# Kernel optimization log

Hardware: AMD Instinct MI355X
Metric: run time of the kernel (lower is better)

The kernel has to match this reference:

```python
import jax, jax.numpy as jnp
import numpy as np

TOPK = 20
EPS = 1e-5  # torch BatchNorm1d default eps


def _segment_softmax(logits, seg, num_segments):
    m = jax.ops.segment_max(logits, seg, num_segments=num_segments)
    e = jnp.exp(logits - m[seg])
    s = jax.ops.segment_sum(e, seg, num_segments=num_segments)
    return e / (s[seg] + 1e-16)


def _forward(data, emb, W_lin, att_i, att_j, att_em_i, att_em_j, bias_gnn,
             W_ff, b_ff, bn1_g, bn1_b, bn2_g, bn2_b, W_out, b_out):
    B, N, F = data.shape
    H, D = att_i.shape
    BN = B * N
    x = data.reshape(BN, F)

    # --- dynamic top-k cosine-similarity graph (original detaches embeddings) ---
    w = jax.lax.stop_gradient(emb)
    nrm = jnp.linalg.norm(w, axis=-1, keepdims=True)  # (N,1)
    cos = (w @ w.T) / (nrm * nrm.T)                   # (N,N)
    _, topk_idx = jax.lax.top_k(cos, TOPK)            # (N,K)

    src = topk_idx.reshape(-1)                        # j (source of message)
    tgt = jnp.repeat(jnp.arange(N), TOPK)             # i (target)
    off = (jnp.arange(B) * N)[:, None]                # batch the edge list
    src_b = (src[None, :] + off).reshape(-1)          # (B*N*K,)
    tgt_b = (tgt[None, :] + off).reshape(-1)
    # remove_self_loops then add_self_loops: mask topk self-edges, append loops
    self_mask = src_b == tgt_b
    loops = jnp.arange(BN)
    src_all = jnp.concatenate([src_b, loops])         # (E,)
    tgt_all = jnp.concatenate([tgt_b, loops])
    dead = jnp.concatenate([self_mask, jnp.zeros(BN, dtype=bool)])

    # --- GraphLayer: GAT-style attention with node embeddings in the keys ---
    xh = (x @ W_lin).reshape(BN, H, D)                # lin(x), per head
    emb_full = jnp.tile(emb, (B, 1))                  # (BN, D) repeated per batch
    # per-node attention scores; key_i = [x_i || emb_i] . [att_i || att_em_i]
    score_i = jnp.einsum('nhd,hd->nh', xh, att_i) + emb_full @ att_em_i.T  # (BN,H)
    score_j = jnp.einsum('nhd,hd->nh', xh, att_j) + emb_full @ att_em_j.T
    alpha = score_i[tgt_all] + score_j[src_all]       # (E,H)
    alpha = jax.nn.leaky_relu(alpha, 0.2)
    alpha = jnp.where(dead[:, None], -1e30, alpha)    # drop removed self-edges
    alpha = _segment_softmax(alpha, tgt_all, BN)      # softmax over in-edges of i
    msgs = xh[src_all] * alpha[:, :, None]            # (E,H,D)
    agg = jax.ops.segment_sum(msgs, tgt_all, num_segments=BN)  # (BN,H,D)
    out = agg.reshape(BN, H * D) + bias_gnn           # concat heads + bias

    # --- GNNLayer head: linear -> BatchNorm1d (train stats) -> relu ---
    out = out @ W_ff + b_ff                           # (BN, D)
    mu = out.mean(0)
    var = out.var(0)
    out = (out - mu) / jnp.sqrt(var + EPS) * bn1_g + bn1_b
    out = jax.nn.relu(out)

    # --- multiply by embeddings, channelwise BN, relu (dropout: eval = identity) ---
    h = out.reshape(B, N, D) * emb[None]              # (B,N,D)
    mu2 = h.mean(axis=(0, 1))
    var2 = h.var(axis=(0, 1))
    h = (h - mu2) / jnp.sqrt(var2 + EPS) * bn2_g + bn2_b
    h = jax.nn.relu(h)

    # --- OutLayer (layer_num=1): single linear per node ---
    return h @ W_out + b_out                          # (B, N, out_win)


def setup_inputs() -> dict:
    key = jax.random.key(0)
    ks = jax.random.split(key, 12)
    B, N, F, D, H, OW = 16, 2000, 128, 64, 4, 200
    s = 0.05
    return {
        'data': jax.random.normal(ks[0], (B, N, F), jnp.float32),
        'emb': jax.random.normal(ks[1], (N, D), jnp.float32),
        'W_lin': jax.random.normal(ks[2], (F, H * D), jnp.float32) * s,
        'att_i': jax.random.normal(ks[3], (H, D), jnp.float32) * s,
        'att_j': jax.random.normal(ks[4], (H, D), jnp.float32) * s,
        'att_em_i': jax.random.normal(ks[5], (H, D), jnp.float32) * s,
        'att_em_j': jax.random.normal(ks[6], (H, D), jnp.float32) * s,
        'bias_gnn': jnp.zeros((H * D,), jnp.float32),
        'W_ff': jax.random.normal(ks[7], (H * D, D), jnp.float32) * s,
        'b_ff': jnp.zeros((D,), jnp.float32),
        'bn1_g': jnp.ones((D,), jnp.float32),
        'bn1_b': jnp.zeros((D,), jnp.float32),
        'bn2_g': jnp.ones((D,), jnp.float32),
        'bn2_b': jnp.zeros((D,), jnp.float32),
        'W_out': jax.random.normal(ks[8], (D, OW), jnp.float32) * s,
        'b_out': jnp.zeros((OW,), jnp.float32),
    }


def reference(data, emb, W_lin, att_i, att_j, att_em_i, att_em_j, bias_gnn,
              W_ff, b_ff, bn1_g, bn1_b, bn2_g, bn2_b, W_out, b_out):
    return _forward(data, emb, W_lin, att_i, att_j, att_em_i, att_em_j, bias_gnn,
                    W_ff, b_ff, bn1_g, bn1_b, bn2_g, bn2_b, W_out, b_out)
```

## Files before the change

### kernel.cpp

```cpp
#include <hip/hip_runtime.h>
#include <math.h>

#define B_   16
#define N_   2000
#define F_   128
#define D_   64
#define H_   4
#define OW_  200
#define K_   20
#define BN_  (B_*N_)
#define HD_  (H_*D_)
#define EPS_ 1e-5f
#define NP_  2048

__global__ __launch_bounds__(256) void k_prep(const float* __restrict__ emb,
                                              const float* __restrict__ biasg,
                                              const float* __restrict__ Wff,
                                              const float* __restrict__ bff,
                                              float* __restrict__ nrm,
                                              float* __restrict__ embT,
                                              float* __restrict__ bias2) {
    const int t = threadIdx.x, b = blockIdx.x;
    const int idx = b * 256 + t;
    {
        int k = idx >> 11, j = idx & (NP_ - 1);
        embT[idx] = (j < N_) ? emb[(size_t)j * D_ + k] : 0.f;
    }
    if (b < 8) {
        int i = idx;
        if (i < N_) {
            const float* e = emb + (size_t)i * D_;
            float s = 0.f;
            #pragma unroll
            for (int d = 0; d < D_; ++d) s += e[d] * e[d];
            nrm[i] = sqrtf(s);
        } else if (i < NP_) {
            nrm[i] = 1.f;
        }
    }
    if (b == 8 && t < D_) {
        float s = bff[t];
        for (int c = 0; c < HD_; ++c) s = fmaf(biasg[c], Wff[(size_t)c * D_ + t], s);
        bias2[t] = s;
    }
}

__global__ __launch_bounds__(256) void k_cos(const float* __restrict__ emb,
                                             const float* __restrict__ embT,
                                             const float* __restrict__ nrm,
                                             float* __restrict__ cosm) {
    const int t    = threadIdx.x;
    const int i0   = blockIdx.y * 16;
    const int r0   = (t >> 6) * 4;
    const int lane = t & 63;
    const int j4   = blockIdx.x * 256 + lane * 4;

    __shared__ float eL[16 * D_];
    for (int idx = t; idx < 16 * D_; idx += 256)
        eL[idx] = emb[(size_t)i0 * D_ + idx];
    __syncthreads();

    float acc[4][4];
    #pragma unroll
    for (int r = 0; r < 4; ++r)
        #pragma unroll
        for (int cc = 0; cc < 4; ++cc) acc[r][cc] = 0.f;

    for (int k4 = 0; k4 < D_; k4 += 4) {
        float es[4][4];
        #pragma unroll
        for (int r = 0; r < 4; ++r) {
            float4 ev = *(const float4*)&eL[(r0 + r) * D_ + k4];
            es[r][0] = ev.x; es[r][1] = ev.y; es[r][2] = ev.z; es[r][3] = ev.w;
        }
        #pragma unroll
        for (int kk = 0; kk < 4; ++kk) {
            float4 b = *(const float4*)&embT[(size_t)(k4 + kk) * NP_ + j4];
            #pragma unroll
            for (int r = 0; r < 4; ++r) {
                acc[r][0] = fmaf(es[r][kk], b.x, acc[r][0]);
                acc[r][1] = fmaf(es[r][kk], b.y, acc[r][1]);
                acc[r][2] = fmaf(es[r][kk], b.z, acc[r][2]);
                acc[r][3] = fmaf(es[r][kk], b.w, acc[r][3]);
            }
        }
    }

    float4 nj = *(const float4*)&nrm[j4];
    #pragma unroll
    for (int r = 0; r < 4; ++r) {
        float ni = nrm[i0 + r0 + r];
        float4 o;
        o.x = acc[r][0] / (ni * nj.x);
        o.y = acc[r][1] / (ni * nj.y);
        o.z = acc[r][2] / (ni * nj.z);
        o.w = acc[r][3] / (ni * nj.w);
        *(float4*)&cosm[(size_t)(i0 + r0 + r) * NP_ + j4] = o;
    }
}

__device__ __forceinline__ unsigned long long kmax64(unsigned long long a,
                                                     unsigned long long b) {
    return a > b ? a : b;
}

__global__ __launch_bounds__(256) void k_sel(const float* __restrict__ cosm,
                                             int* __restrict__ topk) {
    const int t    = threadIdx.x;
    const int lane = t & 63;
    const int i    = blockIdx.x * 4 + (t >> 6);
    const float* row = cosm + (size_t)i * NP_;

    unsigned long long key[32];
    #pragma unroll
    for (int m = 0; m < 8; ++m) {
        float4 b = *(const float4*)&row[m * 256 + lane * 4];
        float vv[4] = {b.x, b.y, b.z, b.w};
        #pragma unroll
        for (int q = 0; q < 4; ++q) {
            const int s = m * 4 + q;
            const int j = m * 256 + lane * 4 + q;
            unsigned int x  = __float_as_uint(vv[q]);
            unsigned int mv = (x & 0x80000000u) ? ~x : (x | 0x80000000u);
            unsigned long long kk =
                ((unsigned long long)mv << 32) | (unsigned int)(NP_ - 1 - j);
            key[s] = (j < N_) ? kk : 0ull;
        }
    }

    unsigned long long loc;
    {
        unsigned long long l1[16];
        #pragma unroll
        for (int s = 0; s < 16; ++s) l1[s] = kmax64(key[s], key[s + 16]);
        unsigned long long l2[8];
        #pragma unroll
        for (int s = 0; s < 8; ++s) l2[s] = kmax64(l1[s], l1[s + 8]);
        unsigned long long l3[4];
        #pragma unroll
        for (int s = 0; s < 4; ++s) l3[s] = kmax64(l2[s], l2[s + 4]);
        loc = kmax64(kmax64(l3[0], l3[2]), kmax64(l3[1], l3[3]));
    }

    for (int k = 0; k < K_; ++k) {
        unsigned long long w = loc;
        #pragma unroll
        for (int off = 1; off < 64; off <<= 1)
            w = kmax64(w, __shfl_xor(w, off, 64));

        if (lane == 0)
            topk[i * K_ + k] = (NP_ - 1) - (int)(unsigned int)(w & 0xFFFFFFFFu);

        #pragma unroll
        for (int s = 0; s < 32; ++s)
            if (key[s] == w) key[s] = 0ull;
        {
            unsigned long long l1[16];
            #pragma unroll
            for (int s = 0; s < 16; ++s) l1[s] = kmax64(key[s], key[s + 16]);
            unsigned long long l2[8];
            #pragma unroll
            for (int s = 0; s < 8; ++s) l2[s] = kmax64(l1[s], l1[s + 8]);
            unsigned long long l3[4];
            #pragma unroll
            for (int s = 0; s < 4; ++s) l3[s] = kmax64(l2[s], l2[s + 4]);
            loc = kmax64(kmax64(l3[0], l3[2]), kmax64(l3[1], l3[3]));
        }
    }
}

__global__ __launch_bounds__(256) void k_lin(const float* __restrict__ x,
                                             const float* __restrict__ Wlin,
                                             const float* __restrict__ emb,
                                             const float* __restrict__ atti,
                                             const float* __restrict__ attj,
                                             const float* __restrict__ attei,
                                             const float* __restrict__ attej,
                                             const float* __restrict__ Wff,
                                             float* __restrict__ yh,
                                             float* __restrict__ si,
                                             float* __restrict__ sj) {
    const int t  = threadIdx.x;
    const int n0 = blockIdx.x * 16;
    const int i0 = n0 % N_;
    const int r0 = (t >> 6) * 4;
    const int lane = t & 63;
    const int c4 = lane * 4;

    __shared__ float xL[16 * F_];
    __shared__ float xhL[16 * HD_];

    for (int idx = t; idx < 16 * F_; idx += 256)
        xL[idx] = x[(size_t)n0 * F_ + idx];
    __syncthreads();

    float acc[4][4];
    #pragma unroll
    for (int r = 0; r < 4; ++r)
        #pragma unroll
        for (int cc = 0; cc < 4; ++cc) acc[r][cc] = 0.f;

    for (int k4 = 0; k4 < F_; k4 += 4) {
        float xs[4][4];
        #pragma unroll
        for (int r = 0; r < 4; ++r) {
            float4 xv = *(const float4*)&xL[(r0 + r) * F_ + k4];
            xs[r][0] = xv.x; xs[r][1] = xv.y; xs[r][2] = xv.z; xs[r][3] = xv.w;
        }
        #pragma unroll
        for (int kk = 0; kk < 4; ++kk) {
            float4 w = *(const float4*)&Wlin[(size_t)(k4 + kk) * HD_ + c4];
            #pragma unroll
            for (int r = 0; r < 4; ++r) {
                acc[r][0] = fmaf(xs[r][kk], w.x, acc[r][0]);
                acc[r][1] = fmaf(xs[r][kk], w.y, acc[r][1]);
                acc[r][2] = fmaf(xs[r][kk], w.z, acc[r][2]);
                acc[r][3] = fmaf(xs[r][kk], w.w, acc[r][3]);
            }
        }
    }

    #pragma unroll
    for (int r = 0; r < 4; ++r) {
        float4 o; o.x = acc[r][0]; o.y = acc[r][1]; o.z = acc[r][2]; o.w = acc[r][3];
        *(float4*)&xhL[(r0 + r) * HD_ + c4] = o;
    }

    {
        const int h  = lane >> 4;
        const int de = 4 * (t & 15);
        float4 ai4  = *(const float4*)&atti[c4];
        float4 aj4  = *(const float4*)&attj[c4];
        float4 aei4 = *(const float4*)&attei[c4];
        float4 aej4 = *(const float4*)&attej[c4];
        #pragma unroll
        for (int r = 0; r < 4; ++r) {
            float4 e4 = *(const float4*)&emb[(size_t)(i0 + r0 + r) * D_ + de];
            float vi = acc[r][0] * ai4.x + e4.x * aei4.x
                     + acc[r][1] * ai4.y + e4.y * aei4.y
                     + acc[r][2] * ai4.z + e4.z * aei4.z
                     + acc[r][3] * ai4.w + e4.w * aei4.w;
            float vj = acc[r][0] * aj4.x + e4.x * aej4.x
                     + acc[r][1] * aj4.y + e4.y * aej4.y
                     + acc[r][2] * aj4.z + e4.z * aej4.z
                     + acc[r][3] * aj4.w + e4.w * aej4.w;
            #pragma unroll
            for (int off = 1; off < 16; off <<= 1) {
                vi += __shfl_xor(vi, off);
                vj += __shfl_xor(vj, off);
            }
            if ((t & 15) == 0) {
                si[(size_t)(n0 + r0 + r) * H_ + h] = vi;
                sj[(size_t)(n0 + r0 + r) * H_ + h] = vj;
            }
        }
    }
    __syncthreads();

    {
        const int h  = c4 >> 6;
        const int d4 = c4 & 63;
        float ya[4][4];
        #pragma unroll
        for (int r = 0; r < 4; ++r)
            #pragma unroll
            for (int cc = 0; cc < 4; ++cc) ya[r][cc] = 0.f;

        for (int k4 = 0; k4 < D_; k4 += 4) {
            float wf[4][4];
            #pragma unroll
            for (int kk = 0; kk < 4; ++kk) {
                float4 w = *(const float4*)&Wff[(size_t)(h * D_ + k4 + kk) * D_ + d4];
                wf[kk][0] = w.x; wf[kk][1] = w.y; wf[kk][2] = w.z; wf[kk][3] = w.w;
            }
            #pragma unroll
            for (int r = 0; r < 4; ++r) {
                float4 xv = *(const float4*)&xhL[(r0 + r) * HD_ + h * D_ + k4];
                ya[r][0] = fmaf(xv.x, wf[0][0], ya[r][0]);
                ya[r][1] = fmaf(xv.x, wf[0][1], ya[r][1]);
                ya[r][2] = fmaf(xv.x, wf[0][2], ya[r][2]);
                ya[r][3] = fmaf(xv.x, wf[0][3], ya[r][3]);
                ya[r][0] = fmaf(xv.y, wf[1][0], ya[r][0]);
                ya[r][1] = fmaf(xv.y, wf[1][1], ya[r][1]);
                ya[r][2] = fmaf(xv.y, wf[1][2], ya[r][2]);
                ya[r][3] = fmaf(xv.y, wf[1][3], ya[r][3]);
                ya[r][0] = fmaf(xv.z, wf[2][0], ya[r][0]);
                ya[r][1] = fmaf(xv.z, wf[2][1], ya[r][1]);
                ya[r][2] = fmaf(xv.z, wf[2][2], ya[r][2]);
                ya[r][3] = fmaf(xv.z, wf[2][3], ya[r][3]);
                ya[r][0] = fmaf(xv.w, wf[3][0], ya[r][0]);
                ya[r][1] = fmaf(xv.w, wf[3][1], ya[r][1]);
                ya[r][2] = fmaf(xv.w, wf[3][2], ya[r][2]);
                ya[r][3] = fmaf(xv.w, wf[3][3], ya[r][3]);
            }
        }
        #pragma unroll
        for (int r = 0; r < 4; ++r) {
            float4 o; o.x = ya[r][0]; o.y = ya[r][1]; o.z = ya[r][2]; o.w = ya[r][3];
            *(float4*)&yh[(size_t)(n0 + r0 + r) * HD_ + c4] = o;
        }
    }
}

#define RA_ 8
__global__ __launch_bounds__(256) void k_attn(const float* __restrict__ yh,
                                              const float* __restrict__ si,
                                              const float* __restrict__ sj,
                                              const int* __restrict__ topk,
                                              const float* __restrict__ bias2,
                                              float* __restrict__ out2) {
    const int t   = threadIdx.x;
    const int nwg = BN_ / RA_;
    const int swz = (blockIdx.x & 7) * (nwg >> 3) + (blockIdx.x >> 3);
    const int n0  = swz * RA_;
    __shared__ int   srcL[RA_][21];
    __shared__ float wA[RA_][H_][21];

    if (t < RA_ * 21) {
        const int r = t / 21, e = t % 21;
        const int n = n0 + r;
        const int i = n % N_;
        const int b = n / N_;
        int s; bool dead = false;
        if (e < K_) { int kk = topk[i * K_ + e]; s = b * N_ + kk; dead = (kk == i); }
        else        { s = n; }
        srcL[r][e] = s;
        #pragma unroll
        for (int h = 0; h < H_; ++h) {
            float a = si[(size_t)n * H_ + h] + sj[(size_t)s * H_ + h];
            a = a > 0.f ? a : 0.2f * a;
            if (dead) a = -1e30f;
            wA[r][h][e] = a;
        }
    }
    __syncthreads();

    if (t < RA_ * H_) {
        const int r = t >> 2, h = t & 3;
        float m = -3e38f;
        for (int e = 0; e < 21; ++e) m = fmaxf(m, wA[r][h][e]);
        float sum = 0.f;
        for (int e = 0; e < 21; ++e) { float ex = expf(wA[r][h][e] - m); wA[r][h][e] = ex; sum += ex; }
        float inv = 1.f / (sum + 1e-16f);
        for (int e = 0; e < 21; ++e) wA[r][h][e] *= inv;
    }
    __syncthreads();

    {
        const int g = t >> 6, lane = t & 63, c4 = lane * 4, h = lane >> 4;
        #pragma unroll
        for (int rr = 0; rr < 2; ++rr) {
            const int r = g * 2 + rr;
            float a0 = 0.f, a1 = 0.f, a2 = 0.f, a3 = 0.f;
            for (int e = 0; e < 21; ++e) {
                float wv = wA[r][h][e];
                float4 yv = *(const float4*)&yh[(size_t)srcL[r][e] * HD_ + c4];
                a0 = fmaf(wv, yv.x, a0); a1 = fmaf(wv, yv.y, a1);
                a2 = fmaf(wv, yv.z, a2); a3 = fmaf(wv, yv.w, a3);
            }
            a0 += __shfl_xor(a0, 16); a0 += __shfl_xor(a0, 32);
            a1 += __shfl_xor(a1, 16); a1 += __shfl_xor(a1, 32);
            a2 += __shfl_xor(a2, 16); a2 += __shfl_xor(a2, 32);
            a3 += __shfl_xor(a3, 16); a3 += __shfl_xor(a3, 32);
            if (lane < 16) {
                float4 b2 = *(const float4*)&bias2[lane * 4];
                float4 o; o.x = a0 + b2.x; o.y = a1 + b2.y;
                          o.z = a2 + b2.z; o.w = a3 + b2.w;
                *(float4*)&out2[(size_t)(n0 + r) * D_ + lane * 4] = o;
            }
        }
    }
}

__global__ __launch_bounds__(256) void k_red1(const float* __restrict__ out2,
                                              double* __restrict__ S,
                                              double* __restrict__ SS) {
    const int t = threadIdx.x;
    double s = 0.0, ss = 0.0;
    const int total = BN_ * D_;
    for (int idx = blockIdx.x * 256 + t; idx < total; idx += gridDim.x * 256) {
        float v = out2[idx];
        s += v; ss += (double)v * v;
    }
    __shared__ double sb[256], ssb[256];
    sb[t] = s; ssb[t] = ss;
    __syncthreads();
    if (t < 64) {
        double a = sb[t] + sb[t + 64] + sb[t + 128] + sb[t + 192];
        double b = ssb[t] + ssb[t + 64] + ssb[t + 128] + ssb[t + 192];
        atomicAdd(&S[t], a);
        atomicAdd(&SS[t], b);
    }
}

__global__ __launch_bounds__(256) void k_bn1(const float* __restrict__ out2,
                                             const float* __restrict__ emb,
                                             const double* __restrict__ S1,
                                             const double* __restrict__ SS1,
                                             const float* __restrict__ g1,
                                             const float* __restrict__ b1,
                                             float* __restrict__ hb,
                                             double* __restrict__ S2,
                                             double* __restrict__ SS2) {
    const int t = threadIdx.x;
    __shared__ float scale[64], shift[64];
    if (t < 64) {
        double mu  = S1[t] / (double)BN_;
        double var = SS1[t] / (double)BN_ - mu * mu;
        float rstd = rsqrtf((float)var + EPS_);
        float sc   = rstd * g1[t];
        scale[t] = sc;
        shift[t] = b1[t] - (float)mu * sc;
    }
    __syncthreads();
    const int d = t & 63;
    double s = 0.0, ss = 0.0;
    const int total = BN_ * D_;
    for (int idx = blockIdx.x * 256 + t; idx < total; idx += gridDim.x * 256) {
        float v = out2[idx];
        v = v * scale[d] + shift[d];
        v = fmaxf(v, 0.f);
        int n = idx >> 6;
        int i = n % N_;
        v *= emb[(size_t)i * D_ + d];
        hb[idx] = v;
        s += v; ss += (double)v * v;
    }
    __shared__ double sb[256], ssb[256];
    sb[t] = s; ssb[t] = ss;
    __syncthreads();
    if (t < 64) {
        double a = sb[t] + sb[t + 64] + sb[t + 128] + sb[t + 192];
        double b = ssb[t] + ssb[t + 64] + ssb[t + 128] + ssb[t + 192];
        atomicAdd(&S2[t], a);
        atomicAdd(&SS2[t], b);
    }
}

__global__ __launch_bounds__(256) void k_out(const float* __restrict__ hb,
                                             const double* __restrict__ S2,
                                             const double* __restrict__ SS2,
                                             const float* __restrict__ g2,
                                             const float* __restrict__ b2,
                                             const float* __restrict__ Wout,
                                             const float* __restrict__ bout,
                                             float* __restrict__ out) {
    const int t  = threadIdx.x;
    const int n0 = blockIdx.x * 16;
    __shared__ float scale[64], shift[64];
    __shared__ float hL[16 * D_];
    if (t < 64) {
        double mu  = S2[t] / (double)BN_;
        double var = SS2[t] / (double)BN_ - mu * mu;
        float rstd = rsqrtf((float)var + EPS_);
        float sc   = rstd * g2[t];
        scale[t] = sc;
        shift[t] = b2[t] - (float)mu * sc;
    }
    __syncthreads();
    for (int idx = t; idx < 16 * D_; idx += 256) {
        float v = hb[(size_t)n0 * D_ + idx];
        int d = idx & 63;
        v = fmaxf(v * scale[d] + shift[d], 0.f);
        hL[idx] = v;
    }
    __syncthreads();
    if (t < OW_) {
        float acc[16];
        #pragma unroll
        for (int r = 0; r < 16; ++r) acc[r] = 0.f;
        for (int d4 = 0; d4 < D_; d4 += 4) {
            float hs[16][4];
            #pragma unroll
            for (int r = 0; r < 16; ++r) {
                float4 hv = *(const float4*)&hL[r * D_ + d4];
                hs[r][0] = hv.x; hs[r][1] = hv.y; hs[r][2] = hv.z; hs[r][3] = hv.w;
            }
            #pragma unroll
            for (int kk = 0; kk < 4; ++kk) {
                float w = Wout[(size_t)(d4 + kk) * OW_ + t];
                #pragma unroll
                for (int r = 0; r < 16; ++r) acc[r] = fmaf(hs[r][kk], w, acc[r]);
            }
        }
        float bo = bout[t];
        #pragma unroll
        for (int r = 0; r < 16; ++r) out[(size_t)(n0 + r) * OW_ + t] = acc[r] + bo;
    }
}

extern "C" void kernel_launch(void* const* d_in, const int* in_sizes, int n_in,
                              void* d_out, int out_size, void* d_ws, size_t ws_size,
                              hipStream_t stream) {
    const float* data  = (const float*)d_in[0];
    const float* emb   = (const float*)d_in[1];
    const float* Wlin  = (const float*)d_in[2];
    const float* atti  = (const float*)d_in[3];
    const float* attj  = (const float*)d_in[4];
    const float* attei = (const float*)d_in[5];
    const float* attej = (const float*)d_in[6];
    const float* biasg = (const float*)d_in[7];
    const float* Wff   = (const float*)d_in[8];
    const float* bff   = (const float*)d_in[9];
    const float* g1    = (const float*)d_in[10];
    const float* b1    = (const float*)d_in[11];
    const float* g2    = (const float*)d_in[12];
    const float* b2    = (const float*)d_in[13];
    const float* Wout  = (const float*)d_in[14];
    const float* bout  = (const float*)d_in[15];
    float* out = (float*)d_out;

    char* w = (char*)d_ws;
    size_t off = 0;
    auto alloc = [&](size_t bytes) -> void* {
        void* p = w + off;
        off += (bytes + 255) & ~(size_t)255;
        return p;
    };
    float*  nrm   = (float*) alloc((size_t)NP_ * sizeof(float));
    int*    topk  = (int*)   alloc((size_t)N_ * K_ * sizeof(int));
    float*  bias2 = (float*) alloc((size_t)D_ * sizeof(float));
    float*  yh   = (float*) alloc((size_t)BN_ * HD_ * sizeof(float));
    float*  embT = yh;
    float*  cosm = yh + (size_t)D_ * NP_;
    float*  si   = (float*) alloc((size_t)BN_ * H_ * sizeof(float));
    float*  sj   = (float*) alloc((size_t)BN_ * H_ * sizeof(float));
    float*  out2 = (float*) alloc((size_t)BN_ * D_ * sizeof(float));
    float*  hb   = (float*) alloc((size_t)BN_ * D_ * sizeof(float));
    double* S1   = (double*)alloc(64 * sizeof(double));
    double* SS1  = (double*)alloc(64 * sizeof(double));
    double* S2   = (double*)alloc(64 * sizeof(double));
    double* SS2  = (double*)alloc(64 * sizeof(double));

    hipMemsetAsync(S1, 0, 4 * 512, stream);

    hipLaunchKernelGGL(k_prep,  dim3(D_*NP_/256),    dim3(256), 0, stream,
                       emb, biasg, Wff, bff, nrm, embT, bias2);
    hipLaunchKernelGGL(k_cos,   dim3(NP_/256, N_/16), dim3(256), 0, stream,
                       emb, embT, nrm, cosm);
    hipLaunchKernelGGL(k_sel,   dim3(N_/4),          dim3(256), 0, stream, cosm, topk);
    hipLaunchKernelGGL(k_lin,   dim3(BN_ / 16),      dim3(256), 0, stream,
                       data, Wlin, emb, atti, attj, attei, attej, Wff, yh, si, sj);
    hipLaunchKernelGGL(k_attn,  dim3(BN_ / RA_),     dim3(256), 0, stream,
                       yh, si, sj, topk, bias2, out2);
    hipLaunchKernelGGL(k_red1,  dim3(512),           dim3(256), 0, stream, out2, S1, SS1);
    hipLaunchKernelGGL(k_bn1,   dim3(512),           dim3(256), 0, stream,
                       out2, emb, S1, SS1, g1, b1, hb, S2, SS2);
    hipLaunchKernelGGL(k_out,   dim3(BN_ / 16),      dim3(256), 0, stream,
                       hb, S2, SS2, g2, b2, Wout, bout, out);
}
```

Measured before the change: 287.3 us.

## Precompose Wlin with per-head Wff and attention vectors to shrink k_lin

Folds the per-head Wff projection into Wlin ahead of time (W2 = Wlin·Wff per head) and precomputes the attention score weights (Wlin·att) and the embedding score terms, all inside the prep kernel. k_lin then does one F×HD GEMM plus a small score dot product instead of two chained GEMMs, an xh staging buffer and shuffle reductions. It also doubles the rows per block to 32 and pads the shared-memory x tile. The reassociation changes floating-point rounding, and the extra prep work is small.

```diff
diff --git a/kernel.cpp b/kernel.cpp
--- a/kernel.cpp
+++ b/kernel.cpp
@@ -14,34 +14,72 @@
 #define NP_  2048
 
 __global__ __launch_bounds__(256) void k_prep(const float* __restrict__ emb,
+                                              const float* __restrict__ Wlin,
+                                              const float* __restrict__ atti,
+                                              const float* __restrict__ attj,
+                                              const float* __restrict__ attei,
+                                              const float* __restrict__ attej,
                                               const float* __restrict__ biasg,
                                               const float* __restrict__ Wff,
                                               const float* __restrict__ bff,
                                               float* __restrict__ nrm,
                                               float* __restrict__ embT,
+                                              float* __restrict__ W2,
+                                              float* __restrict__ wscore,
+                                              float* __restrict__ semb,
                                               float* __restrict__ bias2) {
     const int t = threadIdx.x, b = blockIdx.x;
-    const int idx = b * 256 + t;
-    {
+    if (b < 512) {
+        const int idx = b * 256 + t;
         int k = idx >> 11, j = idx & (NP_ - 1);
         embT[idx] = (j < N_) ? emb[(size_t)j * D_ + k] : 0.f;
-    }
-    if (b < 8) {
-        int i = idx;
+        if (b < 8) {
+            int i = idx;
+            if (i < N_) {
+                const float* e = emb + (size_t)i * D_;
+                float s = 0.f;
+                #pragma unroll
+                for (int d = 0; d < D_; ++d) s += e[d] * e[d];
+                nrm[i] = sqrtf(s);
+            } else if (i < NP_) {
+                nrm[i] = 1.f;
+            }
+        }
+    } else if (b < 640) {
+        const int f = b - 512;
+        const int h = t >> 6, d = t & 63;
+        float s = 0.f;
+        for (int dd = 0; dd < D_; ++dd)
+            s = fmaf(Wlin[(size_t)f * HD_ + h * D_ + dd],
+                     Wff[(size_t)(h * D_ + dd) * D_ + d], s);
+        W2[(size_t)f * HD_ + t] = s;
+    } else if (b < 644) {
+        const int idx = (b - 640) * 256 + t;
+        const int f = idx >> 3, c8 = idx & 7;
+        const int h = c8 & 3;
+        const float* a = (c8 < 4) ? atti : attj;
+        float s = 0.f;
+        for (int d = 0; d < D_; ++d)
+            s = fmaf(Wlin[(size_t)f * HD_ + h * D_ + d], a[h * D_ + d], s);
+        wscore[idx] = s;
+    } else if (b < 707) {
+        const int idx = (b - 644) * 256 + t;
+        const int i = idx >> 3, c8 = idx & 7;
         if (i < N_) {
-            const float* e = emb + (size_t)i * D_;
+            const int h = c8 & 3;
+            const float* a = (c8 < 4) ? attei : attej;
             float s = 0.f;
-            #pragma unroll
-            for (int d = 0; d < D_; ++d) s += e[d] * e[d];
-            nrm[i] = sqrtf(s);
-        } else if (i < NP_) {
-            nrm[i] = 1.f;
-        }
-    }
-    if (b == 8 && t < D_) {
-        float s = bff[t];
-        for (int c = 0; c < HD_; ++c) s = fmaf(biasg[c], Wff[(size_t)c * D_ + t], s);
-        bias2[t] = s;
+            for (int d = 0; d < D_; ++d)
+                s = fmaf(emb[(size_t)i * D_ + d], a[h * D_ + d], s);
+            semb[idx] = s;
+        }
+    } else {
+        if (t < D_) {
+            float s = bff[t];
+            for (int c = 0; c < HD_; ++c)
+                s = fmaf(biasg[c], Wff[(size_t)c * D_ + t], s);
+            bias2[t] = s;
+        }
     }
 }
 
@@ -169,49 +207,47 @@
     }
 }
 
+#define XS_ 132
 __global__ __launch_bounds__(256) void k_lin(const float* __restrict__ x,
-                                             const float* __restrict__ Wlin,
-                                             const float* __restrict__ emb,
-                                             const float* __restrict__ atti,
-                                             const float* __restrict__ attj,
-                                             const float* __restrict__ attei,
-                                             const float* __restrict__ attej,
-                                             const float* __restrict__ Wff,
+                                             const float* __restrict__ W2,
+                                             const float* __restrict__ wscore,
+                                             const float* __restrict__ semb,
                                              float* __restrict__ yh,
                                              float* __restrict__ si,
                                              float* __restrict__ sj) {
-    const int t  = threadIdx.x;
-    const int n0 = blockIdx.x * 16;
-    const int i0 = n0 % N_;
-    const int r0 = (t >> 6) * 4;
+    const int t    = threadIdx.x;
+    const int n0   = blockIdx.x * 32;
+    const int r0   = (t >> 6) * 8;
     const int lane = t & 63;
-    const int c4 = lane * 4;
-
-    __shared__ float xL[16 * F_];
-    __shared__ float xhL[16 * HD_];
-
-    for (int idx = t; idx < 16 * F_; idx += 256)
-        xL[idx] = x[(size_t)n0 * F_ + idx];
-    __syncthreads();
-
-    float acc[4][4];
+    const int c4   = lane * 4;
+
+    __shared__ float xL[32 * XS_];
+    __shared__ float wsL[F_ * 8];
+
+    for (int idx = t; idx < 32 * F_; idx += 256)
+        xL[(idx >> 7) * XS_ + (idx & 127)] = x[(size_t)n0 * F_ + idx];
+    for (int idx = t; idx < F_ * 8; idx += 256)
+        wsL[idx] = wscore[idx];
+    __syncthreads();
+
+    float acc[8][4];
     #pragma unroll
-    for (int r = 0; r < 4; ++r)
+    for (int r = 0; r < 8; ++r)
         #pragma unroll
         for (int cc = 0; cc < 4; ++cc) acc[r][cc] = 0.f;
 
     for (int k4 = 0; k4 < F_; k4 += 4) {
-        float xs[4][4];
-        #pragma unroll
-        for (int r = 0; r < 4; ++r) {
-            float4 xv = *(const float4*)&xL[(r0 + r) * F_ + k4];
+        float xs[8][4];
+        #pragma unroll
+        for (int r = 0; r < 8; ++r) {
+            float4 xv = *(const float4*)&xL[(r0 + r) * XS_ + k4];
             xs[r][0] = xv.x; xs[r][1] = xv.y; xs[r][2] = xv.z; xs[r][3] = xv.w;
         }
         #pragma unroll
         for (int kk = 0; kk < 4; ++kk) {
-            float4 w = *(const float4*)&Wlin[(size_t)(k4 + kk) * HD_ + c4];
-            #pragma unroll
-            for (int r = 0; r < 4; ++r) {
+            float4 w = *(const float4*)&W2[(size_t)(k4 + kk) * HD_ + c4];
+            #pragma unroll
+            for (int r = 0; r < 8; ++r) {
                 acc[r][0] = fmaf(xs[r][kk], w.x, acc[r][0]);
                 acc[r][1] = fmaf(xs[r][kk], w.y, acc[r][1]);
                 acc[r][2] = fmaf(xs[r][kk], w.z, acc[r][2]);
@@ -221,84 +257,26 @@
     }
 
     #pragma unroll
-    for (int r = 0; r < 4; ++r) {
+    for (int r = 0; r < 8; ++r) {
         float4 o; o.x = acc[r][0]; o.y = acc[r][1]; o.z = acc[r][2]; o.w = acc[r][3];
-        *(float4*)&xhL[(r0 + r) * HD_ + c4] = o;
+        *(float4*)&yh[(size_t)(n0 + r0 + r) * HD_ + c4] = o;
     }
 
     {
-        const int h  = lane >> 4;
-        const int de = 4 * (t & 15);
-        float4 ai4  = *(const float4*)&atti[c4];
-        float4 aj4  = *(const float4*)&attj[c4];
-        float4 aei4 = *(const float4*)&attei[c4];
-        float4 aej4 = *(const float4*)&attej[c4];
-        #pragma unroll
-        for (int r = 0; r < 4; ++r) {
-            float4 e4 = *(const float4*)&emb[(size_t)(i0 + r0 + r) * D_ + de];
-            float vi = acc[r][0] * ai4.x + e4.x * aei4.x
-                     + acc[r][1] * ai4.y + e4.y * aei4.y
-                     + acc[r][2] * ai4.z + e4.z * aei4.z
-                     + acc[r][3] * ai4.w + e4.w * aei4.w;
-            float vj = acc[r][0] * aj4.x + e4.x * aej4.x
-                     + acc[r][1] * aj4.y + e4.y * aej4.y
-                     + acc[r][2] * aj4.z + e4.z * aej4.z
-                     + acc[r][3] * aj4.w + e4.w * aej4.w;
-            #pragma unroll
-            for (int off = 1; off < 16; off <<= 1) {
-                vi += __shfl_xor(vi, off);
-                vj += __shfl_xor(vj, off);
-            }
-            if ((t & 15) == 0) {
-                si[(size_t)(n0 + r0 + r) * H_ + h] = vi;
-                sj[(size_t)(n0 + r0 + r) * H_ + h] = vj;
-            }
-        }
-    }
-    __syncthreads();
-
-    {
-        const int h  = c4 >> 6;
-        const int d4 = c4 & 63;
-        float ya[4][4];
-        #pragma unroll
-        for (int r = 0; r < 4; ++r)
-            #pragma unroll
-            for (int cc = 0; cc < 4; ++cc) ya[r][cc] = 0.f;
-
-        for (int k4 = 0; k4 < D_; k4 += 4) {
-            float wf[4][4];
-            #pragma unroll
-            for (int kk = 0; kk < 4; ++kk) {
-                float4 w = *(const float4*)&Wff[(size_t)(h * D_ + k4 + kk) * D_ + d4];
-                wf[kk][0] = w.x; wf[kk][1] = w.y; wf[kk][2] = w.z; wf[kk][3] = w.w;
-            }
-            #pragma unroll
-            for (int r = 0; r < 4; ++r) {
-                float4 xv = *(const float4*)&xhL[(r0 + r) * HD_ + h * D_ + k4];
-                ya[r][0] = fmaf(xv.x, wf[0][0], ya[r][0]);
-                ya[r][1] = fmaf(xv.x, wf[0][1], ya[r][1]);
-                ya[r][2] = fmaf(xv.x, wf[0][2], ya[r][2]);
-                ya[r][3] = fmaf(xv.x, wf[0][3], ya[r][3]);
-                ya[r][0] = fmaf(xv.y, wf[1][0], ya[r][0]);
-                ya[r][1] = fmaf(xv.y, wf[1][1], ya[r][1]);
-                ya[r][2] = fmaf(xv.y, wf[1][2], ya[r][2]);
-                ya[r][3] = fmaf(xv.y, wf[1][3], ya[r][3]);
-                ya[r][0] = fmaf(xv.z, wf[2][0], ya[r][0]);
-                ya[r][1] = fmaf(xv.z, wf[2][1], ya[r][1]);
-                ya[r][2] = fmaf(xv.z, wf[2][2], ya[r][2]);
-                ya[r][3] = fmaf(xv.z, wf[2][3], ya[r][3]);
-                ya[r][0] = fmaf(xv.w, wf[3][0], ya[r][0]);
-                ya[r][1] = fmaf(xv.w, wf[3][1], ya[r][1]);
-                ya[r][2] = fmaf(xv.w, wf[3][2], ya[r][2]);
-                ya[r][3] = fmaf(xv.w, wf[3][3], ya[r][3]);
-            }
-        }
-        #pragma unroll
-        for (int r = 0; r < 4; ++r) {
-            float4 o; o.x = ya[r][0]; o.y = ya[r][1]; o.z = ya[r][2]; o.w = ya[r][3];
-            *(float4*)&yh[(size_t)(n0 + r0 + r) * HD_ + c4] = o;
-        }
+        const int row = t >> 3, c8 = t & 7;
+        float s = 0.f;
+        for (int k4 = 0; k4 < F_; k4 += 4) {
+            float4 xv = *(const float4*)&xL[row * XS_ + k4];
+            s = fmaf(xv.x, wsL[(k4 + 0) * 8 + c8], s);
+            s = fmaf(xv.y, wsL[(k4 + 1) * 8 + c8], s);
+            s = fmaf(xv.z, wsL[(k4 + 2) * 8 + c8], s);
+            s = fmaf(xv.w, wsL[(k4 + 3) * 8 + c8], s);
+        }
+        const int n = n0 + row;
+        const int i = n % N_;
+        s += semb[i * 8 + c8];
+        if (c8 < 4) si[(size_t)n * H_ + c8]       = s;
+        else        sj[(size_t)n * H_ + (c8 - 4)] = s;
     }
 }
 
@@ -517,9 +495,12 @@
         off += (bytes + 255) & ~(size_t)255;
         return p;
     };
-    float*  nrm   = (float*) alloc((size_t)NP_ * sizeof(float));
-    int*    topk  = (int*)   alloc((size_t)N_ * K_ * sizeof(int));
-    float*  bias2 = (float*) alloc((size_t)D_ * sizeof(float));
+    float*  nrm    = (float*) alloc((size_t)NP_ * sizeof(float));
+    int*    topk   = (int*)   alloc((size_t)N_ * K_ * sizeof(int));
+    float*  bias2  = (float*) alloc((size_t)D_ * sizeof(float));
+    float*  W2     = (float*) alloc((size_t)F_ * HD_ * sizeof(float));
+    float*  wscore = (float*) alloc((size_t)F_ * 8 * sizeof(float));
+    float*  semb   = (float*) alloc((size_t)N_ * 8 * sizeof(float));
     float*  yh   = (float*) alloc((size_t)BN_ * HD_ * sizeof(float));
     float*  embT = yh;
     float*  cosm = yh + (size_t)D_ * NP_;
@@ -534,13 +515,14 @@
 
     hipMemsetAsync(S1, 0, 4 * 512, stream);
 
-    hipLaunchKernelGGL(k_prep,  dim3(D_*NP_/256),    dim3(256), 0, stream,
-                       emb, biasg, Wff, bff, nrm, embT, bias2);
+    hipLaunchKernelGGL(k_prep,  dim3(708),          dim3(256), 0, stream,
+                       emb, Wlin, atti, attj, attei, attej, biasg, Wff, bff,
+                       nrm, embT, W2, wscore, semb, bias2);
     hipLaunchKernelGGL(k_cos,   dim3(NP_/256, N_/16), dim3(256), 0, stream,
                        emb, embT, nrm, cosm);
     hipLaunchKernelGGL(k_sel,   dim3(N_/4),          dim3(256), 0, stream, cosm, topk);
-    hipLaunchKernelGGL(k_lin,   dim3(BN_ / 16),      dim3(256), 0, stream,
-                       data, Wlin, emb, atti, attj, attei, attej, Wff, yh, si, sj);
+    hipLaunchKernelGGL(k_lin,   dim3(BN_ / 32),      dim3(256), 0, stream,
+                       data, W2, wscore, semb, yh, si, sj);
     hipLaunchKernelGGL(k_attn,  dim3(BN_ / RA_),     dim3(256), 0, stream,
                        yh, si, sj, topk, bias2, out2);
     hipLaunchKernelGGL(k_red1,  dim3(512),           dim3(256), 0, stream, out2, S1, SS1);
```

After: 262.9 us. -8.5%, faster.
